# Optimization experiments

Measured on AMD Instinct MI355X. Metric: run time of the kernel, lower is better.

The kernel has to match this reference:

```python
import jax, jax.numpy as jnp
import numpy as np
import math

N = 100000   # nodes
E = 500000   # edges
IN_C = 128
EDGE_D = 64
HEADS = 4
OUT_C = 32
HC = HEADS * OUT_C  # 128


def setup_inputs() -> dict:
    key = jax.random.key(0)
    ks = jax.random.split(key, 12)
    s_in = 1.0 / math.sqrt(IN_C)
    s_e = 1.0 / math.sqrt(EDGE_D)
    return {
        "x": jax.random.normal(ks[0], (N, IN_C), jnp.float32),
        "edge_index": jax.random.randint(ks[1], (2, E), 0, N, dtype=jnp.int32),
        "edge_attr": jax.random.normal(ks[2], (E, EDGE_D), jnp.float32),
        "Wq": jax.random.uniform(ks[3], (HC, IN_C), jnp.float32, -s_in, s_in),
        "bq": jax.random.uniform(ks[4], (HC,), jnp.float32, -s_in, s_in),
        "Wk": jax.random.uniform(ks[5], (HC, IN_C), jnp.float32, -s_in, s_in),
        "bk": jax.random.uniform(ks[6], (HC,), jnp.float32, -s_in, s_in),
        "Wv": jax.random.uniform(ks[7], (HC, IN_C), jnp.float32, -s_in, s_in),
        "bv": jax.random.uniform(ks[8], (HC,), jnp.float32, -s_in, s_in),
        "We": jax.random.uniform(ks[9], (HC, EDGE_D), jnp.float32, -s_e, s_e),
        "Ws": jax.random.uniform(ks[10], (HC, IN_C), jnp.float32, -s_in, s_in),
        "bs": jax.random.uniform(ks[11], (HC,), jnp.float32, -s_in, s_in),
    }


def reference(x, edge_index, edge_attr, Wq, bq, Wk, bk, Wv, bv, We, Ws, bs):
    src = edge_index[0]
    dst = edge_index[1]
    x_i = x[dst]                       # [E, IN_C] target-node feats
    x_j = x[src]                       # [E, IN_C] source-node feats

    e = (edge_attr @ We.T).reshape(E, HEADS, OUT_C)
    q = (x_i @ Wq.T + bq).reshape(E, HEADS, OUT_C)
    k = (x_j @ Wk.T + bk).reshape(E, HEADS, OUT_C) + e

    alpha = jnp.sum(q * k, axis=-1) / jnp.sqrt(jnp.float32(OUT_C))  # [E, H]
    # Faithful to the source: GLOBAL per-column max (not per-segment), then
    # segment-sum of exponentials over destination nodes.
    m = jnp.max(alpha, axis=0)                                      # [H]
    exp_a = jnp.exp(alpha - m)                                      # [E, H]
    denom = jax.ops.segment_sum(exp_a, dst, num_segments=N)         # [N, H]
    alpha = exp_a / (denom[dst] + 1e-16)                            # [E, H]

    v = (x_j @ Wv.T + bv).reshape(E, HEADS, OUT_C) + e
    msg = v * alpha[:, :, None]                                     # [E, H, C]

    out = jax.ops.segment_sum(msg.reshape(E, HC), dst, num_segments=N)  # [N, HC]
    out = out + (x @ Ws.T + bs)
    return out
```

## Files before the change

kernel.cpp:

```cpp
#include <hip/hip_runtime.h>
#include <hip/hip_bf16.h>
#include <math.h>

#define N_NODES 100000
#define N_EDGES 500000
#define M0 8.0f
#define INV_SQRT32 0.17677669529663687f
#define NB_SCAN 98

typedef __attribute__((ext_vector_type(8))) short bf16x8;
typedef __attribute__((ext_vector_type(4))) float f32x4;
typedef __attribute__((ext_vector_type(8))) unsigned short us8;

static __device__ __forceinline__ unsigned short f2bf(float f) {
    __hip_bfloat16 h = __float2bfloat16(f);
    return *(unsigned short*)&h;
}

__global__ __launch_bounds__(256) void prep_w_kernel(
    const float* __restrict__ Wq, const float* __restrict__ Wk,
    const float* __restrict__ Wv, const float* __restrict__ Ws,
    const float* __restrict__ We,
    unsigned short* __restrict__ WBh, unsigned short* __restrict__ WBl,
    unsigned short* __restrict__ WEh, unsigned short* __restrict__ WEl)
{
    const int i = blockIdx.x * 256 + threadIdx.x;
    float v;
    unsigned short *ph, *pl;
    int idx;
    if (i < 65536) {
        const int p = i >> 14;
        const float* W = (p == 0) ? Wq : (p == 1) ? Wk : (p == 2) ? Wv : Ws;
        v = W[i & 16383];
        ph = WBh; pl = WBl; idx = i;
    } else if (i < 73728) {
        idx = i - 65536;
        v = We[idx];
        ph = WEh; pl = WEl;
    } else {
        return;
    }
    const unsigned short h = f2bf(v);
    ph[idx] = h;
    pl[idx] = f2bf(v - __uint_as_float((unsigned)h << 16));
}

__global__ __launch_bounds__(256) void node_proj_mfma(
    const float* __restrict__ x,
    const unsigned short* __restrict__ WBh, const unsigned short* __restrict__ WBl,
    const float* __restrict__ bq, const float* __restrict__ bk,
    const float* __restrict__ bv, const float* __restrict__ bs,
    float* __restrict__ Qn, float* __restrict__ Kn, float* __restrict__ Vn,
    float* __restrict__ out)
{
    __shared__ __align__(16) unsigned short xh[64 * 128];
    __shared__ __align__(16) unsigned short xl[64 * 128];
    __shared__ __align__(16) unsigned short wh[128 * 64];
    __shared__ __align__(16) unsigned short wl[128 * 64];

    const int t = threadIdx.x;
    const long r0 = (long)blockIdx.x * 64;
    const int lane = t & 63;
    const int wid = t >> 6;
    const int fr = lane & 15;
    const int fq = lane >> 4;

    for (int i = t; i < 64 * 32; i += 256) {
        const int r = i >> 5;
        const int s = i & 31;
        const long row = r0 + r;
        float4 v = (row < N_NODES) ? *(const float4*)&x[row * 128 + s * 4]
                                   : make_float4(0.f, 0.f, 0.f, 0.f);
        const unsigned short h0 = f2bf(v.x), h1 = f2bf(v.y),
                             h2 = f2bf(v.z), h3 = f2bf(v.w);
        ushort4 hv, lv;
        hv.x = h0; hv.y = h1; hv.z = h2; hv.w = h3;
        lv.x = f2bf(v.x - __uint_as_float((unsigned)h0 << 16));
        lv.y = f2bf(v.y - __uint_as_float((unsigned)h1 << 16));
        lv.z = f2bf(v.z - __uint_as_float((unsigned)h2 << 16));
        lv.w = f2bf(v.w - __uint_as_float((unsigned)h3 << 16));
        const int di = r * 128 + ((s * 4) ^ ((r & 7) << 3));
        *(ushort4*)&xh[di] = hv;
        *(ushort4*)&xl[di] = lv;
    }

    for (int p = 0; p < 4; ++p) {
        const float* bias = (p == 0) ? bq : (p == 1) ? bk : (p == 2) ? bv : bs;
        float* dst        = (p == 0) ? Qn : (p == 1) ? Kn : (p == 2) ? Vn : out;

        f32x4 acc[4][2];
#pragma unroll
        for (int m = 0; m < 4; ++m)
#pragma unroll
            for (int n = 0; n < 2; ++n) acc[m][n] = (f32x4){0.f, 0.f, 0.f, 0.f};

        for (int kc = 0; kc < 2; ++kc) {
            __syncthreads();
            for (int i = t; i < 1024; i += 256) {
                const int r = i >> 3;
                const int s = i & 7;
                const int gi = p * 16384 + r * 128 + kc * 64 + s * 8;
                const int di = r * 64 + ((s * 8) ^ ((r & 7) << 3));
                *(us8*)&wh[di] = *(const us8*)&WBh[gi];
                *(us8*)&wl[di] = *(const us8*)&WBl[gi];
            }
            __syncthreads();

#pragma unroll
            for (int ks = 0; ks < 2; ++ks) {
                const int kx = kc * 64 + ks * 32 + fq * 8;
                const int kw = ks * 32 + fq * 8;
                bf16x8 ah[4], al[4], bh[2], bl[2];
#pragma unroll
                for (int m = 0; m < 4; ++m) {
                    const int r = m * 16 + fr;
                    const int di = r * 128 + (kx ^ ((r & 7) << 3));
                    ah[m] = *(const bf16x8*)&xh[di];
                    al[m] = *(const bf16x8*)&xl[di];
                }
#pragma unroll
                for (int n = 0; n < 2; ++n) {
                    const int r = wid * 32 + n * 16 + fr;
                    const int di = r * 64 + (kw ^ ((r & 7) << 3));
                    bh[n] = *(const bf16x8*)&wh[di];
                    bl[n] = *(const bf16x8*)&wl[di];
                }
#pragma unroll
                for (int m = 0; m < 4; ++m)
#pragma unroll
                    for (int n = 0; n < 2; ++n) {
                        acc[m][n] = __builtin_amdgcn_mfma_f32_16x16x32_bf16(
                            ah[m], bh[n], acc[m][n], 0, 0, 0);
                        acc[m][n] = __builtin_amdgcn_mfma_f32_16x16x32_bf16(
                            ah[m], bl[n], acc[m][n], 0, 0, 0);
                        acc[m][n] = __builtin_amdgcn_mfma_f32_16x16x32_bf16(
                            al[m], bh[n], acc[m][n], 0, 0, 0);
                    }
            }
        }

        float bb[2];
#pragma unroll
        for (int n = 0; n < 2; ++n) bb[n] = bias[wid * 32 + n * 16 + fr];
#pragma unroll
        for (int m = 0; m < 4; ++m) {
            const long rowb = r0 + m * 16 + fq * 4;
#pragma unroll
            for (int j = 0; j < 4; ++j) {
                if (rowb + j < N_NODES) {
#pragma unroll
                    for (int n = 0; n < 2; ++n)
                        dst[(rowb + j) * 128 + wid * 32 + n * 16 + fr] =
                            acc[m][n][j] + bb[n];
                }
            }
        }
    }
}

__global__ __launch_bounds__(256) void ee_gemm_mfma(
    const float* __restrict__ ea,
    const unsigned short* __restrict__ WEh, const unsigned short* __restrict__ WEl,
    unsigned short* __restrict__ Ee)
{
    __shared__ __align__(16) unsigned short eh[128 * 64];
    __shared__ __align__(16) unsigned short el[128 * 64];
    __shared__ __align__(16) unsigned short wh[128 * 64];
    __shared__ __align__(16) unsigned short wl[128 * 64];

    const int t = threadIdx.x;
    const long e0 = (long)blockIdx.x * 128;
    const int lane = t & 63;
    const int wr = (t >> 6) >> 1;
    const int wc = (t >> 6) & 1;
    const int fr = lane & 15;
    const int fq = lane >> 4;

    for (int i = t; i < 1024; i += 256) {
        const int r = i >> 3;
        const int s = i & 7;
        const int di = r * 64 + ((s * 8) ^ ((r & 7) << 3));
        *(us8*)&wh[di] = *(const us8*)&WEh[r * 64 + s * 8];
        *(us8*)&wl[di] = *(const us8*)&WEl[r * 64 + s * 8];
    }
    for (int i = t; i < 128 * 16; i += 256) {
        const int r = i >> 4;
        const int s = i & 15;
        const long e = e0 + r;
        float4 v = (e < N_EDGES) ? *(const float4*)&ea[e * 64 + s * 4]
                                 : make_float4(0.f, 0.f, 0.f, 0.f);
        const unsigned short h0 = f2bf(v.x), h1 = f2bf(v.y),
                             h2 = f2bf(v.z), h3 = f2bf(v.w);
        ushort4 hv, lv;
        hv.x = h0; hv.y = h1; hv.z = h2; hv.w = h3;
        lv.x = f2bf(v.x - __uint_as_float((unsigned)h0 << 16));
        lv.y = f2bf(v.y - __uint_as_float((unsigned)h1 << 16));
        lv.z = f2bf(v.z - __uint_as_float((unsigned)h2 << 16));
        lv.w = f2bf(v.w - __uint_as_float((unsigned)h3 << 16));
        const int di = r * 64 + ((s * 4) ^ ((r & 7) << 3));
        *(ushort4*)&eh[di] = hv;
        *(ushort4*)&el[di] = lv;
    }
    __syncthreads();

    f32x4 acc[4][4];
#pragma unroll
    for (int m = 0; m < 4; ++m)
#pragma unroll
        for (int n = 0; n < 4; ++n) acc[m][n] = (f32x4){0.f, 0.f, 0.f, 0.f};

#pragma unroll
    for (int ks = 0; ks < 2; ++ks) {
        const int kk = ks * 32 + fq * 8;
        bf16x8 ah[4], al[4], bh[4], bl[4];
#pragma unroll
        for (int m = 0; m < 4; ++m) {
            const int r = wr * 64 + m * 16 + fr;
            const int di = r * 64 + (kk ^ ((r & 7) << 3));
            ah[m] = *(const bf16x8*)&eh[di];
            al[m] = *(const bf16x8*)&el[di];
        }
#pragma unroll
        for (int n = 0; n < 4; ++n) {
            const int r = wc * 64 + n * 16 + fr;
            const int di = r * 64 + (kk ^ ((r & 7) << 3));
            bh[n] = *(const bf16x8*)&wh[di];
            bl[n] = *(const bf16x8*)&wl[di];
        }
#pragma unroll
        for (int m = 0; m < 4; ++m)
#pragma unroll
            for (int n = 0; n < 4; ++n) {
                acc[m][n] = __builtin_amdgcn_mfma_f32_16x16x32_bf16(
                    ah[m], bh[n], acc[m][n], 0, 0, 0);
                acc[m][n] = __builtin_amdgcn_mfma_f32_16x16x32_bf16(
                    ah[m], bl[n], acc[m][n], 0, 0, 0);
                acc[m][n] = __builtin_amdgcn_mfma_f32_16x16x32_bf16(
                    al[m], bh[n], acc[m][n], 0, 0, 0);
            }
    }

#pragma unroll
    for (int m = 0; m < 4; ++m) {
        const long erow = e0 + wr * 64 + m * 16 + fq * 4;
#pragma unroll
        for (int j = 0; j < 4; ++j) {
            if (erow + j < N_EDGES) {
#pragma unroll
                for (int n = 0; n < 4; ++n)
                    Ee[(erow + j) * 128 + wc * 64 + n * 16 + fr] =
                        f2bf(acc[m][n][j]);
            }
        }
    }
}

__global__ __launch_bounds__(256) void csr_hist_kernel(
    const int* __restrict__ ei, int* __restrict__ cursor)
{
    const int e = blockIdx.x * 256 + threadIdx.x;
    if (e >= N_EDGES) return;
    atomicAdd(&cursor[ei[N_EDGES + e]], 1);
}

__global__ __launch_bounds__(256) void csr_scan_part_kernel(
    const int* __restrict__ deg, int* __restrict__ bsum)
{
    __shared__ int red[256];
    const int t = threadIdx.x;
    const int i0 = blockIdx.x * 1024 + t * 4;
    int s = 0;
#pragma unroll
    for (int j = 0; j < 4; ++j) {
        const int n = i0 + j;
        if (n < N_NODES) s += deg[n];
    }
    red[t] = s;
    __syncthreads();
    for (int o = 128; o > 0; o >>= 1) {
        if (t < o) red[t] += red[t + o];
        __syncthreads();
    }
    if (t == 0) bsum[blockIdx.x] = red[0];
}

__global__ void csr_scan_top_kernel(int* __restrict__ bsum, int* __restrict__ csr_off)
{
    if (threadIdx.x == 0 && blockIdx.x == 0) {
        int run = 0;
        for (int b = 0; b < NB_SCAN; ++b) {
            const int v = bsum[b];
            bsum[b] = run;
            run += v;
        }
        csr_off[N_NODES] = run;
    }
}

__global__ __launch_bounds__(256) void csr_scan_final_kernel(
    const int* __restrict__ bsum, int* __restrict__ cursor,
    int* __restrict__ csr_off)
{
    __shared__ int ts[256];
    const int t = threadIdx.x;
    const int i0 = blockIdx.x * 1024 + t * 4;
    int d[4];
    int s = 0;
#pragma unroll
    for (int j = 0; j < 4; ++j) {
        const int n = i0 + j;
        d[j] = (n < N_NODES) ? cursor[n] : 0;
        s += d[j];
    }
    ts[t] = s;
    __syncthreads();
    for (int o = 1; o < 256; o <<= 1) {
        int v = (t >= o) ? ts[t - o] : 0;
        __syncthreads();
        ts[t] += v;
        __syncthreads();
    }
    int run = bsum[blockIdx.x] + ts[t] - s;
#pragma unroll
    for (int j = 0; j < 4; ++j) {
        const int n = i0 + j;
        if (n < N_NODES) {
            csr_off[n] = run;
            cursor[n] = run;
            run += d[j];
        }
    }
}

__global__ __launch_bounds__(256) void csr_fill_kernel(
    const int* __restrict__ ei, int* __restrict__ cursor,
    int* __restrict__ csr_eid, int* __restrict__ csr_src)
{
    const int e = blockIdx.x * 256 + threadIdx.x;
    if (e >= N_EDGES) return;
    const int dst = ei[N_EDGES + e];
    const int pos = atomicAdd(&cursor[dst], 1);
    csr_eid[pos] = e;
    csr_src[pos] = ei[e];
}

__global__ __launch_bounds__(256) void fused_attn_kernel(
    const int* __restrict__ csr_off, const int* __restrict__ csr_eid,
    const int* __restrict__ csr_src, const unsigned short* __restrict__ Ee,
    const float* __restrict__ Qn, const float* __restrict__ Kn,
    const float* __restrict__ Vn, float* __restrict__ out)
{
    const int lane = threadIdx.x & 63;
    const int l2 = lane * 2;
    const long n = (long)blockIdx.x * 4 + (threadIdx.x >> 6);

    const int off0 = csr_off[n];
    const int off1 = csr_off[n + 1];
    const float2 q = *(const float2*)&Qn[n * 128 + l2];
    float2 acc = *(const float2*)&out[n * 128 + l2];

    float dsum = 0.f;
    for (int base = off0; base < off1; base += 64) {
        const int cnt = min(64, off1 - base);
        int eid = 0, src = 0;
        if (base + lane < off1) {
            eid = csr_eid[base + lane];
            src = csr_src[base + lane];
        }
        for (int j = 0; j < cnt; ++j) {
            const long e = __shfl(eid, j, 64);
            const long s = __shfl(src, j, 64);
            const unsigned u = *(const unsigned*)&Ee[e * 128 + l2];
            const float2 k = *(const float2*)&Kn[s * 128 + l2];
            float p = q.x * (k.x + __uint_as_float(u << 16)) +
                      q.y * (k.y + __uint_as_float(u & 0xffff0000u));
#pragma unroll
            for (int o = 1; o < 16; o <<= 1) p += __shfl_xor(p, o, 64);
            dsum += __expf(p * INV_SQRT32 - M0);
        }
    }
    const float rd = 1.f / (dsum + 1e-16f);

    for (int base = off0; base < off1; base += 64) {
        const int cnt = min(64, off1 - base);
        int eid = 0, src = 0;
        if (base + lane < off1) {
            eid = csr_eid[base + lane];
            src = csr_src[base + lane];
        }
        for (int j = 0; j < cnt; ++j) {
            const long e = __shfl(eid, j, 64);
            const long s = __shfl(src, j, 64);
            const unsigned u = *(const unsigned*)&Ee[e * 128 + l2];
            const float2 k = *(const float2*)&Kn[s * 128 + l2];
            const float ea0 = __uint_as_float(u << 16);
            const float ea1 = __uint_as_float(u & 0xffff0000u);
            float p = q.x * (k.x + ea0) + q.y * (k.y + ea1);
#pragma unroll
            for (int o = 1; o < 16; o <<= 1) p += __shfl_xor(p, o, 64);
            const float an = __expf(p * INV_SQRT32 - M0) * rd;
            const float2 v = *(const float2*)&Vn[s * 128 + l2];
            acc.x = fmaf(v.x + ea0, an, acc.x);
            acc.y = fmaf(v.y + ea1, an, acc.y);
        }
    }
    *(float2*)&out[n * 128 + l2] = acc;
}

extern "C" void kernel_launch(void* const* d_in, const int* in_sizes, int n_in,
                              void* d_out, int out_size, void* d_ws, size_t ws_size,
                              hipStream_t stream)
{
    const float* x  = (const float*)d_in[0];
    const int*   ei = (const int*)d_in[1];
    const float* ea = (const float*)d_in[2];
    const float* Wq = (const float*)d_in[3];
    const float* bq = (const float*)d_in[4];
    const float* Wk = (const float*)d_in[5];
    const float* bk = (const float*)d_in[6];
    const float* Wv = (const float*)d_in[7];
    const float* bv = (const float*)d_in[8];
    const float* We = (const float*)d_in[9];
    const float* Ws = (const float*)d_in[10];
    const float* bs = (const float*)d_in[11];
    float* out = (float*)d_out;

    float* ws = (float*)d_ws;
    float* Qn = ws;
    float* Kn = ws + 12800000;
    float* Vn = ws + 25600000;
    int* csr_off = (int*)(ws + 38400000);
    int* cursor  = (int*)(ws + 38500004);
    int* csr_eid = (int*)(ws + 38600004);
    int* csr_src = (int*)(ws + 39100004);
    int* bsum    = (int*)(ws + 39600004);
    unsigned short* WBh = (unsigned short*)(ws + 40000000);
    unsigned short* WBl = (unsigned short*)(ws + 40050000);
    unsigned short* WEh = (unsigned short*)(ws + 40100000);
    unsigned short* WEl = (unsigned short*)(ws + 40110000);
    unsigned short* Ee = (unsigned short*)((char*)d_ws + 163200032);

    hipMemsetAsync(cursor, 0, N_NODES * sizeof(int), stream);

    prep_w_kernel<<<288, 256, 0, stream>>>(Wq, Wk, Wv, Ws, We, WBh, WBl, WEh, WEl);

    node_proj_mfma<<<1563, 256, 0, stream>>>(x, WBh, WBl, bq, bk, bv, bs,
                                             Qn, Kn, Vn, out);
    ee_gemm_mfma<<<3907, 256, 0, stream>>>(ea, WEh, WEl, Ee);

    csr_hist_kernel<<<(N_EDGES + 255) / 256, 256, 0, stream>>>(ei, cursor);
    csr_scan_part_kernel<<<NB_SCAN, 256, 0, stream>>>(cursor, bsum);
    csr_scan_top_kernel<<<1, 64, 0, stream>>>(bsum, csr_off);
    csr_scan_final_kernel<<<NB_SCAN, 256, 0, stream>>>(bsum, cursor, csr_off);
    csr_fill_kernel<<<(N_EDGES + 255) / 256, 256, 0, stream>>>(ei, cursor, csr_eid, csr_src);

    fused_attn_kernel<<<25000, 256, 0, stream>>>(csr_off, csr_eid, csr_src, Ee,
                                                 Qn, Kn, Vn, out);
}
```

Before: 644.3 us.

## Merge projection, edge GEMM and histogram into one launch; single-pass attention

Folds the memset into the weight-prep kernel and merges the node-projection GEMM, the edge-attribute GEMM and the degree histogram into one heterogeneous kernel that dispatches on block index. The three-kernel CSR scan becomes a single 1024-thread block scan. The attention kernel now does one pass over incoming edges, accumulating the unnormalised numerator and the denominator together and normalising at the end, so the Kn/Ee gathers are no longer repeated. This cuts launch count and halves the edge gather traffic, at the cost of a single-block scan and mixed workloads sharing one grid.

```diff
diff --git a/kernel.cpp b/kernel.cpp
--- a/kernel.cpp
+++ b/kernel.cpp
@@ -6,7 +6,11 @@
 #define N_EDGES 500000
 #define M0 8.0f
 #define INV_SQRT32 0.17677669529663687f
-#define NB_SCAN 98
+
+#define NB_HIST 1954
+#define NB_PROJ 1563
+#define NB_EE   3907
+#define GRID_MEGA (NB_HIST + NB_PROJ + NB_EE)
 
 typedef __attribute__((ext_vector_type(8))) short bf16x8;
 typedef __attribute__((ext_vector_type(4))) float f32x4;
@@ -17,317 +21,281 @@
     return *(unsigned short*)&h;
 }
 
-__global__ __launch_bounds__(256) void prep_w_kernel(
+static __device__ __forceinline__ void split4(float4 v, ushort4& hv, ushort4& lv) {
+    const unsigned short h0 = f2bf(v.x), h1 = f2bf(v.y),
+                         h2 = f2bf(v.z), h3 = f2bf(v.w);
+    hv.x = h0; hv.y = h1; hv.z = h2; hv.w = h3;
+    lv.x = f2bf(v.x - __uint_as_float((unsigned)h0 << 16));
+    lv.y = f2bf(v.y - __uint_as_float((unsigned)h1 << 16));
+    lv.z = f2bf(v.z - __uint_as_float((unsigned)h2 << 16));
+    lv.w = f2bf(v.w - __uint_as_float((unsigned)h3 << 16));
+}
+
+__global__ __launch_bounds__(256) void prep_kernel(
     const float* __restrict__ Wq, const float* __restrict__ Wk,
     const float* __restrict__ Wv, const float* __restrict__ Ws,
     const float* __restrict__ We,
     unsigned short* __restrict__ WBh, unsigned short* __restrict__ WBl,
-    unsigned short* __restrict__ WEh, unsigned short* __restrict__ WEl)
+    unsigned short* __restrict__ WEh, unsigned short* __restrict__ WEl,
+    int* __restrict__ cursor)
 {
     const int i = blockIdx.x * 256 + threadIdx.x;
-    float v;
-    unsigned short *ph, *pl;
-    int idx;
+    if (i < N_NODES) cursor[i] = 0;
     if (i < 65536) {
         const int p = i >> 14;
         const float* W = (p == 0) ? Wq : (p == 1) ? Wk : (p == 2) ? Wv : Ws;
-        v = W[i & 16383];
-        ph = WBh; pl = WBl; idx = i;
+        const float v = W[i & 16383];
+        const unsigned short h = f2bf(v);
+        WBh[i] = h;
+        WBl[i] = f2bf(v - __uint_as_float((unsigned)h << 16));
     } else if (i < 73728) {
-        idx = i - 65536;
-        v = We[idx];
-        ph = WEh; pl = WEl;
-    } else {
-        return;
-    }
-    const unsigned short h = f2bf(v);
-    ph[idx] = h;
-    pl[idx] = f2bf(v - __uint_as_float((unsigned)h << 16));
-}
-
-__global__ __launch_bounds__(256) void node_proj_mfma(
-    const float* __restrict__ x,
+        const int idx = i - 65536;
+        const float v = We[idx];
+        const unsigned short h = f2bf(v);
+        WEh[idx] = h;
+        WEl[idx] = f2bf(v - __uint_as_float((unsigned)h << 16));
+    }
+}
+
+__global__ __launch_bounds__(256) void mega_kernel(
+    const float* __restrict__ x, const int* __restrict__ ei,
+    const float* __restrict__ ea,
     const unsigned short* __restrict__ WBh, const unsigned short* __restrict__ WBl,
+    const unsigned short* __restrict__ WEh, const unsigned short* __restrict__ WEl,
     const float* __restrict__ bq, const float* __restrict__ bk,
     const float* __restrict__ bv, const float* __restrict__ bs,
     float* __restrict__ Qn, float* __restrict__ Kn, float* __restrict__ Vn,
-    float* __restrict__ out)
-{
-    __shared__ __align__(16) unsigned short xh[64 * 128];
-    __shared__ __align__(16) unsigned short xl[64 * 128];
-    __shared__ __align__(16) unsigned short wh[128 * 64];
-    __shared__ __align__(16) unsigned short wl[128 * 64];
+    float* __restrict__ out, unsigned short* __restrict__ Ee,
+    int* __restrict__ cursor)
+{
+    __shared__ __align__(16) unsigned short sAh[8192];
+    __shared__ __align__(16) unsigned short sAl[8192];
+    __shared__ __align__(16) unsigned short sWh[8192];
+    __shared__ __align__(16) unsigned short sWl[8192];
 
     const int t = threadIdx.x;
-    const long r0 = (long)blockIdx.x * 64;
+    const int bid = blockIdx.x;
+
+    if (bid < NB_HIST) {
+        const int e = bid * 256 + t;
+        if (e < N_EDGES) atomicAdd(&cursor[ei[N_EDGES + e]], 1);
+        return;
+    }
+
+    const int lane = t & 63;
+    const int fr = lane & 15;
+    const int fq = lane >> 4;
+
+    if (bid < NB_HIST + NB_PROJ) {
+        const long r0 = (long)(bid - NB_HIST) * 64;
+        const int wid = t >> 6;
+
+        for (int i = t; i < 2048; i += 256) {
+            const int r = i >> 5;
+            const int k4 = (i & 31) * 4;
+            const long row = r0 + r;
+            float4 v = (row < N_NODES) ? *(const float4*)&x[row * 128 + k4]
+                                       : make_float4(0.f, 0.f, 0.f, 0.f);
+            ushort4 hv, lv; split4(v, hv, lv);
+            const int di = r * 128 + (k4 ^ ((r & 7) << 3));
+            *(ushort4*)&sAh[di] = hv;
+            *(ushort4*)&sAl[di] = lv;
+        }
+
+        for (int p = 0; p < 4; ++p) {
+            const float* bias = (p == 0) ? bq : (p == 1) ? bk : (p == 2) ? bv : bs;
+            float* dst        = (p == 0) ? Qn : (p == 1) ? Kn : (p == 2) ? Vn : out;
+
+            f32x4 acc[4][2];
+#pragma unroll
+            for (int m = 0; m < 4; ++m)
+#pragma unroll
+                for (int n = 0; n < 2; ++n) acc[m][n] = (f32x4){0.f, 0.f, 0.f, 0.f};
+
+            for (int kc = 0; kc < 2; ++kc) {
+                __syncthreads();
+                for (int i = t; i < 1024; i += 256) {
+                    const int r = i >> 3;
+                    const int s = i & 7;
+                    const int gi = p * 16384 + r * 128 + kc * 64 + s * 8;
+                    const int di = r * 64 + ((s * 8) ^ ((r & 7) << 3));
+                    *(us8*)&sWh[di] = *(const us8*)&WBh[gi];
+                    *(us8*)&sWl[di] = *(const us8*)&WBl[gi];
+                }
+                __syncthreads();
+
+#pragma unroll
+                for (int ks = 0; ks < 2; ++ks) {
+                    const int kx = kc * 64 + ks * 32 + fq * 8;
+                    const int kw = ks * 32 + fq * 8;
+                    bf16x8 ah[4], al[4], bh[2], bl[2];
+#pragma unroll
+                    for (int m = 0; m < 4; ++m) {
+                        const int r = m * 16 + fr;
+                        const int di = r * 128 + (kx ^ ((r & 7) << 3));
+                        ah[m] = *(const bf16x8*)&sAh[di];
+                        al[m] = *(const bf16x8*)&sAl[di];
+                    }
+#pragma unroll
+                    for (int n = 0; n < 2; ++n) {
+                        const int r = wid * 32 + n * 16 + fr;
+                        const int di = r * 64 + (kw ^ ((r & 7) << 3));
+                        bh[n] = *(const bf16x8*)&sWh[di];
+                        bl[n] = *(const bf16x8*)&sWl[di];
+                    }
+#pragma unroll
+                    for (int m = 0; m < 4; ++m)
+#pragma unroll
+                        for (int n = 0; n < 2; ++n) {
+                            acc[m][n] = __builtin_amdgcn_mfma_f32_16x16x32_bf16(
+                                ah[m], bh[n], acc[m][n], 0, 0, 0);
+                            acc[m][n] = __builtin_amdgcn_mfma_f32_16x16x32_bf16(
+                                ah[m], bl[n], acc[m][n], 0, 0, 0);
+                            acc[m][n] = __builtin_amdgcn_mfma_f32_16x16x32_bf16(
+                                al[m], bh[n], acc[m][n], 0, 0, 0);
+                        }
+                }
+            }
+
+            float bb[2];
+#pragma unroll
+            for (int n = 0; n < 2; ++n) bb[n] = bias[wid * 32 + n * 16 + fr];
+#pragma unroll
+            for (int m = 0; m < 4; ++m) {
+                const long rowb = r0 + m * 16 + fq * 4;
+#pragma unroll
+                for (int j = 0; j < 4; ++j) {
+                    if (rowb + j < N_NODES) {
+#pragma unroll
+                        for (int n = 0; n < 2; ++n)
+                            dst[(rowb + j) * 128 + wid * 32 + n * 16 + fr] =
+                                acc[m][n][j] + bb[n];
+                    }
+                }
+            }
+        }
+    } else {
+        const long e0 = (long)(bid - NB_HIST - NB_PROJ) * 128;
+        const int wr = (t >> 6) >> 1;
+        const int wc = (t >> 6) & 1;
+
+        for (int i = t; i < 1024; i += 256) {
+            const int r = i >> 3;
+            const int s = i & 7;
+            const int di = r * 64 + ((s * 8) ^ ((r & 7) << 3));
+            *(us8*)&sWh[di] = *(const us8*)&WEh[r * 64 + s * 8];
+            *(us8*)&sWl[di] = *(const us8*)&WEl[r * 64 + s * 8];
+        }
+        for (int i = t; i < 2048; i += 256) {
+            const int r = i >> 4;
+            const int k4 = (i & 15) * 4;
+            const long e = e0 + r;
+            float4 v = (e < N_EDGES) ? *(const float4*)&ea[e * 64 + k4]
+                                     : make_float4(0.f, 0.f, 0.f, 0.f);
+            ushort4 hv, lv; split4(v, hv, lv);
+            const int di = r * 64 + (k4 ^ ((r & 7) << 3));
+            *(ushort4*)&sAh[di] = hv;
+            *(ushort4*)&sAl[di] = lv;
+        }
+        __syncthreads();
+
+        f32x4 acc[4][4];
+#pragma unroll
+        for (int m = 0; m < 4; ++m)
+#pragma unroll
+            for (int n = 0; n < 4; ++n) acc[m][n] = (f32x4){0.f, 0.f, 0.f, 0.f};
+
+#pragma unroll
+        for (int ks = 0; ks < 2; ++ks) {
+            const int kk = ks * 32 + fq * 8;
+            bf16x8 ah[4], al[4], bh[4], bl[4];
+#pragma unroll
+            for (int m = 0; m < 4; ++m) {
+                const int r = wr * 64 + m * 16 + fr;
+                const int di = r * 64 + (kk ^ ((r & 7) << 3));
+                ah[m] = *(const bf16x8*)&sAh[di];
+                al[m] = *(const bf16x8*)&sAl[di];
+            }
+#pragma unroll
+            for (int n = 0; n < 4; ++n) {
+                const int r = wc * 64 + n * 16 + fr;
+                const int di = r * 64 + (kk ^ ((r & 7) << 3));
+                bh[n] = *(const bf16x8*)&sWh[di];
+                bl[n] = *(const bf16x8*)&sWl[di];
+            }
+#pragma unroll
+            for (int m = 0; m < 4; ++m)
+#pragma unroll
+                for (int n = 0; n < 4; ++n) {
+                    acc[m][n] = __builtin_amdgcn_mfma_f32_16x16x32_bf16(
+                        ah[m], bh[n], acc[m][n], 0, 0, 0);
+                    acc[m][n] = __builtin_amdgcn_mfma_f32_16x16x32_bf16(
+                        ah[m], bl[n], acc[m][n], 0, 0, 0);
+                    acc[m][n] = __builtin_amdgcn_mfma_f32_16x16x32_bf16(
+                        al[m], bh[n], acc[m][n], 0, 0, 0);
+                }
+        }
+
+#pragma unroll
+        for (int m = 0; m < 4; ++m) {
+            const long erow = e0 + wr * 64 + m * 16 + fq * 4;
+#pragma unroll
+            for (int j = 0; j < 4; ++j) {
+                if (erow + j < N_EDGES) {
+#pragma unroll
+                    for (int n = 0; n < 4; ++n)
+                        Ee[(erow + j) * 128 + wc * 64 + n * 16 + fr] =
+                            f2bf(acc[m][n][j]);
+                }
+            }
+        }
+    }
+}
+
+__global__ __launch_bounds__(1024) void csr_scan_kernel(
+    int* __restrict__ cursor, int* __restrict__ csr_off)
+{
+    __shared__ int wsum[16];
+    const int t = threadIdx.x;
     const int lane = t & 63;
     const int wid = t >> 6;
-    const int fr = lane & 15;
-    const int fq = lane >> 4;
-
-    for (int i = t; i < 64 * 32; i += 256) {
-        const int r = i >> 5;
-        const int s = i & 31;
-        const long row = r0 + r;
-        float4 v = (row < N_NODES) ? *(const float4*)&x[row * 128 + s * 4]
-                                   : make_float4(0.f, 0.f, 0.f, 0.f);
-        const unsigned short h0 = f2bf(v.x), h1 = f2bf(v.y),
-                             h2 = f2bf(v.z), h3 = f2bf(v.w);
-        ushort4 hv, lv;
-        hv.x = h0; hv.y = h1; hv.z = h2; hv.w = h3;
-        lv.x = f2bf(v.x - __uint_as_float((unsigned)h0 << 16));
-        lv.y = f2bf(v.y - __uint_as_float((unsigned)h1 << 16));
-        lv.z = f2bf(v.z - __uint_as_float((unsigned)h2 << 16));
-        lv.w = f2bf(v.w - __uint_as_float((unsigned)h3 << 16));
-        const int di = r * 128 + ((s * 4) ^ ((r & 7) << 3));
-        *(ushort4*)&xh[di] = hv;
-        *(ushort4*)&xl[di] = lv;
-    }
-
-    for (int p = 0; p < 4; ++p) {
-        const float* bias = (p == 0) ? bq : (p == 1) ? bk : (p == 2) ? bv : bs;
-        float* dst        = (p == 0) ? Qn : (p == 1) ? Kn : (p == 2) ? Vn : out;
-
-        f32x4 acc[4][2];
-#pragma unroll
-        for (int m = 0; m < 4; ++m)
-#pragma unroll
-            for (int n = 0; n < 2; ++n) acc[m][n] = (f32x4){0.f, 0.f, 0.f, 0.f};
-
-        for (int kc = 0; kc < 2; ++kc) {
-            __syncthreads();
-            for (int i = t; i < 1024; i += 256) {
-                const int r = i >> 3;
-                const int s = i & 7;
-                const int gi = p * 16384 + r * 128 + kc * 64 + s * 8;
-                const int di = r * 64 + ((s * 8) ^ ((r & 7) << 3));
-                *(us8*)&wh[di] = *(const us8*)&WBh[gi];
-                *(us8*)&wl[di] = *(const us8*)&WBl[gi];
-            }
-            __syncthreads();
-
-#pragma unroll
-            for (int ks = 0; ks < 2; ++ks) {
-                const int kx = kc * 64 + ks * 32 + fq * 8;
-                const int kw = ks * 32 + fq * 8;
-                bf16x8 ah[4], al[4], bh[2], bl[2];
-#pragma unroll
-                for (int m = 0; m < 4; ++m) {
-                    const int r = m * 16 + fr;
-                    const int di = r * 128 + (kx ^ ((r & 7) << 3));
-                    ah[m] = *(const bf16x8*)&xh[di];
-                    al[m] = *(const bf16x8*)&xl[di];
-                }
-#pragma unroll
-                for (int n = 0; n < 2; ++n) {
-                    const int r = wid * 32 + n * 16 + fr;
-                    const int di = r * 64 + (kw ^ ((r & 7) << 3));
-                    bh[n] = *(const bf16x8*)&wh[di];
-                    bl[n] = *(const bf16x8*)&wl[di];
-                }
-#pragma unroll
-                for (int m = 0; m < 4; ++m)
-#pragma unroll
-                    for (int n = 0; n < 2; ++n) {
-                        acc[m][n] = __builtin_amdgcn_mfma_f32_16x16x32_bf16(
-                            ah[m], bh[n], acc[m][n], 0, 0, 0);
-                        acc[m][n] = __builtin_amdgcn_mfma_f32_16x16x32_bf16(
-                            ah[m], bl[n], acc[m][n], 0, 0, 0);
-                        acc[m][n] = __builtin_amdgcn_mfma_f32_16x16x32_bf16(
-                            al[m], bh[n], acc[m][n], 0, 0, 0);
-                    }
-            }
-        }
-
-        float bb[2];
-#pragma unroll
-        for (int n = 0; n < 2; ++n) bb[n] = bias[wid * 32 + n * 16 + fr];
-#pragma unroll
-        for (int m = 0; m < 4; ++m) {
-            const long rowb = r0 + m * 16 + fq * 4;
-#pragma unroll
-            for (int j = 0; j < 4; ++j) {
-                if (rowb + j < N_NODES) {
-#pragma unroll
-                    for (int n = 0; n < 2; ++n)
-                        dst[(rowb + j) * 128 + wid * 32 + n * 16 + fr] =
-                            acc[m][n][j] + bb[n];
-                }
-            }
-        }
-    }
-}
-
-__global__ __launch_bounds__(256) void ee_gemm_mfma(
-    const float* __restrict__ ea,
-    const unsigned short* __restrict__ WEh, const unsigned short* __restrict__ WEl,
-    unsigned short* __restrict__ Ee)
-{
-    __shared__ __align__(16) unsigned short eh[128 * 64];
-    __shared__ __align__(16) unsigned short el[128 * 64];
-    __shared__ __align__(16) unsigned short wh[128 * 64];
-    __shared__ __align__(16) unsigned short wl[128 * 64];
-
-    const int t = threadIdx.x;
-    const long e0 = (long)blockIdx.x * 128;
-    const int lane = t & 63;
-    const int wr = (t >> 6) >> 1;
-    const int wc = (t >> 6) & 1;
-    const int fr = lane & 15;
-    const int fq = lane >> 4;
-
-    for (int i = t; i < 1024; i += 256) {
-        const int r = i >> 3;
-        const int s = i & 7;
-        const int di = r * 64 + ((s * 8) ^ ((r & 7) << 3));
-        *(us8*)&wh[di] = *(const us8*)&WEh[r * 64 + s * 8];
-        *(us8*)&wl[di] = *(const us8*)&WEl[r * 64 + s * 8];
-    }
-    for (int i = t; i < 128 * 16; i += 256) {
-        const int r = i >> 4;
-        const int s = i & 15;
-        const long e = e0 + r;
-        float4 v = (e < N_EDGES) ? *(const float4*)&ea[e * 64 + s * 4]
-                                 : make_float4(0.f, 0.f, 0.f, 0.f);
-        const unsigned short h0 = f2bf(v.x), h1 = f2bf(v.y),
-                             h2 = f2bf(v.z), h3 = f2bf(v.w);
-        ushort4 hv, lv;
-        hv.x = h0; hv.y = h1; hv.z = h2; hv.w = h3;
-        lv.x = f2bf(v.x - __uint_as_float((unsigned)h0 << 16));
-        lv.y = f2bf(v.y - __uint_as_float((unsigned)h1 << 16));
-        lv.z = f2bf(v.z - __uint_as_float((unsigned)h2 << 16));
-        lv.w = f2bf(v.w - __uint_as_float((unsigned)h3 << 16));
-        const int di = r * 64 + ((s * 4) ^ ((r & 7) << 3));
-        *(ushort4*)&eh[di] = hv;
-        *(ushort4*)&el[di] = lv;
-    }
+    const int n0 = t * 100;
+    const bool active = (t < 1000);
+
+    int tsum = 0;
+    if (active) {
+        for (int q = 0; q < 25; ++q) {
+            const int4 d = *(const int4*)&cursor[n0 + q * 4];
+            tsum += d.x + d.y + d.z + d.w;
+        }
+    }
+    int inc = tsum;
+#pragma unroll
+    for (int o = 1; o < 64; o <<= 1) {
+        const int v = __shfl_up(inc, o, 64);
+        if (lane >= o) inc += v;
+    }
+    if (lane == 63) wsum[wid] = inc;
     __syncthreads();
-
-    f32x4 acc[4][4];
-#pragma unroll
-    for (int m = 0; m < 4; ++m)
-#pragma unroll
-        for (int n = 0; n < 4; ++n) acc[m][n] = (f32x4){0.f, 0.f, 0.f, 0.f};
-
-#pragma unroll
-    for (int ks = 0; ks < 2; ++ks) {
-        const int kk = ks * 32 + fq * 8;
-        bf16x8 ah[4], al[4], bh[4], bl[4];
-#pragma unroll
-        for (int m = 0; m < 4; ++m) {
-            const int r = wr * 64 + m * 16 + fr;
-            const int di = r * 64 + (kk ^ ((r & 7) << 3));
-            ah[m] = *(const bf16x8*)&eh[di];
-            al[m] = *(const bf16x8*)&el[di];
-        }
-#pragma unroll
-        for (int n = 0; n < 4; ++n) {
-            const int r = wc * 64 + n * 16 + fr;
-            const int di = r * 64 + (kk ^ ((r & 7) << 3));
-            bh[n] = *(const bf16x8*)&wh[di];
-            bl[n] = *(const bf16x8*)&wl[di];
-        }
-#pragma unroll
-        for (int m = 0; m < 4; ++m)
-#pragma unroll
-            for (int n = 0; n < 4; ++n) {
-                acc[m][n] = __builtin_amdgcn_mfma_f32_16x16x32_bf16(
-                    ah[m], bh[n], acc[m][n], 0, 0, 0);
-                acc[m][n] = __builtin_amdgcn_mfma_f32_16x16x32_bf16(
-                    ah[m], bl[n], acc[m][n], 0, 0, 0);
-                acc[m][n] = __builtin_amdgcn_mfma_f32_16x16x32_bf16(
-                    al[m], bh[n], acc[m][n], 0, 0, 0);
-            }
-    }
-
-#pragma unroll
-    for (int m = 0; m < 4; ++m) {
-        const long erow = e0 + wr * 64 + m * 16 + fq * 4;
-#pragma unroll
-        for (int j = 0; j < 4; ++j) {
-            if (erow + j < N_EDGES) {
-#pragma unroll
-                for (int n = 0; n < 4; ++n)
-                    Ee[(erow + j) * 128 + wc * 64 + n * 16 + fr] =
-                        f2bf(acc[m][n][j]);
-            }
-        }
-    }
-}
-
-__global__ __launch_bounds__(256) void csr_hist_kernel(
-    const int* __restrict__ ei, int* __restrict__ cursor)
-{
-    const int e = blockIdx.x * 256 + threadIdx.x;
-    if (e >= N_EDGES) return;
-    atomicAdd(&cursor[ei[N_EDGES + e]], 1);
-}
-
-__global__ __launch_bounds__(256) void csr_scan_part_kernel(
-    const int* __restrict__ deg, int* __restrict__ bsum)
-{
-    __shared__ int red[256];
-    const int t = threadIdx.x;
-    const int i0 = blockIdx.x * 1024 + t * 4;
-    int s = 0;
-#pragma unroll
-    for (int j = 0; j < 4; ++j) {
-        const int n = i0 + j;
-        if (n < N_NODES) s += deg[n];
-    }
-    red[t] = s;
+    if (t == 0) {
+        int run = 0;
+#pragma unroll
+        for (int w = 0; w < 16; ++w) { const int v = wsum[w]; wsum[w] = run; run += v; }
+        csr_off[N_NODES] = run;
+    }
     __syncthreads();
-    for (int o = 128; o > 0; o >>= 1) {
-        if (t < o) red[t] += red[t + o];
-        __syncthreads();
-    }
-    if (t == 0) bsum[blockIdx.x] = red[0];
-}
-
-__global__ void csr_scan_top_kernel(int* __restrict__ bsum, int* __restrict__ csr_off)
-{
-    if (threadIdx.x == 0 && blockIdx.x == 0) {
-        int run = 0;
-        for (int b = 0; b < NB_SCAN; ++b) {
-            const int v = bsum[b];
-            bsum[b] = run;
-            run += v;
-        }
-        csr_off[N_NODES] = run;
-    }
-}
-
-__global__ __launch_bounds__(256) void csr_scan_final_kernel(
-    const int* __restrict__ bsum, int* __restrict__ cursor,
-    int* __restrict__ csr_off)
-{
-    __shared__ int ts[256];
-    const int t = threadIdx.x;
-    const int i0 = blockIdx.x * 1024 + t * 4;
-    int d[4];
-    int s = 0;
-#pragma unroll
-    for (int j = 0; j < 4; ++j) {
-        const int n = i0 + j;
-        d[j] = (n < N_NODES) ? cursor[n] : 0;
-        s += d[j];
-    }
-    ts[t] = s;
-    __syncthreads();
-    for (int o = 1; o < 256; o <<= 1) {
-        int v = (t >= o) ? ts[t - o] : 0;
-        __syncthreads();
-        ts[t] += v;
-        __syncthreads();
-    }
-    int run = bsum[blockIdx.x] + ts[t] - s;
-#pragma unroll
-    for (int j = 0; j < 4; ++j) {
-        const int n = i0 + j;
-        if (n < N_NODES) {
-            csr_off[n] = run;
-            cursor[n] = run;
-            run += d[j];
+    if (active) {
+        int run = wsum[wid] + inc - tsum;
+        for (int q = 0; q < 25; ++q) {
+            const int n = n0 + q * 4;
+            const int4 d = *(const int4*)&cursor[n];
+            int4 offv;
+            offv.x = run; run += d.x;
+            offv.y = run; run += d.y;
+            offv.z = run; run += d.z;
+            offv.w = run; run += d.w;
+            *(int4*)&csr_off[n] = offv;
+            *(int4*)&cursor[n]  = offv;
         }
     }
 }
@@ -357,30 +325,9 @@
     const int off0 = csr_off[n];
     const int off1 = csr_off[n + 1];
     const float2 q = *(const float2*)&Qn[n * 128 + l2];
-    float2 acc = *(const float2*)&out[n * 128 + l2];
 
     float dsum = 0.f;
-    for (int base = off0; base < off1; base += 64) {
-        const int cnt = min(64, off1 - base);
-        int eid = 0, src = 0;
-        if (base + lane < off1) {
-            eid = csr_eid[base + lane];
-            src = csr_src[base + lane];
-        }
-        for (int j = 0; j < cnt; ++j) {
-            const long e = __shfl(eid, j, 64);
-            const long s = __shfl(src, j, 64);
-            const unsigned u = *(const unsigned*)&Ee[e * 128 + l2];
-            const float2 k = *(const float2*)&Kn[s * 128 + l2];
-            float p = q.x * (k.x + __uint_as_float(u << 16)) +
-                      q.y * (k.y + __uint_as_float(u & 0xffff0000u));
-#pragma unroll
-            for (int o = 1; o < 16; o <<= 1) p += __shfl_xor(p, o, 64);
-            dsum += __expf(p * INV_SQRT32 - M0);
-        }
-    }
-    const float rd = 1.f / (dsum + 1e-16f);
-
+    float2 acc = make_float2(0.f, 0.f);
     for (int base = off0; base < off1; base += 64) {
         const int cnt = min(64, off1 - base);
         int eid = 0, src = 0;
@@ -398,13 +345,18 @@
             float p = q.x * (k.x + ea0) + q.y * (k.y + ea1);
 #pragma unroll
             for (int o = 1; o < 16; o <<= 1) p += __shfl_xor(p, o, 64);
-            const float an = __expf(p * INV_SQRT32 - M0) * rd;
+            const float an = __expf(p * INV_SQRT32 - M0);
+            dsum += an;
             const float2 v = *(const float2*)&Vn[s * 128 + l2];
             acc.x = fmaf(v.x + ea0, an, acc.x);
             acc.y = fmaf(v.y + ea1, an, acc.y);
         }
     }
-    *(float2*)&out[n * 128 + l2] = acc;
+    const float rd = 1.f / (dsum + 1e-16f);
+    float2 o = *(const float2*)&out[n * 128 + l2];
+    o.x = fmaf(acc.x, rd, o.x);
+    o.y = fmaf(acc.y, rd, o.y);
+    *(float2*)&out[n * 128 + l2] = o;
 }
 
 extern "C" void kernel_launch(void* const* d_in, const int* in_sizes, int n_in,
@@ -433,26 +385,23 @@
     int* cursor  = (int*)(ws + 38500004);
     int* csr_eid = (int*)(ws + 38600004);
     int* csr_src = (int*)(ws + 39100004);
-    int* bsum    = (int*)(ws + 39600004);
     unsigned short* WBh = (unsigned short*)(ws + 40000000);
     unsigned short* WBl = (unsigned short*)(ws + 40050000);
     unsigned short* WEh = (unsigned short*)(ws + 40100000);
     unsigned short* WEl = (unsigned short*)(ws + 40110000);
     unsigned short* Ee = (unsigned short*)((char*)d_ws + 163200032);
 
-    hipMemsetAsync(cursor, 0, N_NODES * sizeof(int), stream);
-
-    prep_w_kernel<<<288, 256, 0, stream>>>(Wq, Wk, Wv, Ws, We, WBh, WBl, WEh, WEl);
-
-    node_proj_mfma<<<1563, 256, 0, stream>>>(x, WBh, WBl, bq, bk, bv, bs,
-                                             Qn, Kn, Vn, out);
-    ee_gemm_mfma<<<3907, 256, 0, stream>>>(ea, WEh, WEl, Ee);
-
-    csr_hist_kernel<<<(N_EDGES + 255) / 256, 256, 0, stream>>>(ei, cursor);
-    csr_scan_part_kernel<<<NB_SCAN, 256, 0, stream>>>(cursor, bsum);
-    csr_scan_top_kernel<<<1, 64, 0, stream>>>(bsum, csr_off);
-    csr_scan_final_kernel<<<NB_SCAN, 256, 0, stream>>>(bsum, cursor, csr_off);
-    csr_fill_kernel<<<(N_EDGES + 255) / 256, 256, 0, stream>>>(ei, cursor, csr_eid, csr_src);
+    prep_kernel<<<391, 256, 0, stream>>>(Wq, Wk, Wv, Ws, We,
+                                         WBh, WBl, WEh, WEl, cursor);
+
+    mega_kernel<<<GRID_MEGA, 256, 0, stream>>>(x, ei, ea,
+                                               WBh, WBl, WEh, WEl,
+                                               bq, bk, bv, bs,
+                                               Qn, Kn, Vn, out, Ee, cursor);
+
+    csr_scan_kernel<<<1, 1024, 0, stream>>>(cursor, csr_off);
+
+    csr_fill_kernel<<<NB_HIST, 256, 0, stream>>>(ei, cursor, csr_eid, csr_src);
 
     fused_attn_kernel<<<25000, 256, 0, stream>>>(csr_off, csr_eid, csr_src, Ee,
                                                  Qn, Kn, Vn, out);
```

New measurement: 599.6 us. 6.9% less time.
